# Kernel optimization log

Measured on AMD Instinct MI355X. Metric: run time of the kernel, lower is better.

The kernel has to match this reference:

```python
import jax, jax.numpy as jnp
import numpy as np

B, LQ, LK = 16, 1024, 4096
QD, KD = 512, 512


def setup_inputs() -> dict:
    key = jax.random.key(0)
    ks = jax.random.split(key, 8)
    s = lambda d: 1.0 / np.sqrt(d)
    return {
        "query": jax.random.normal(ks[0], (B, LQ, QD), dtype=jnp.float32),
        "keys": jax.random.normal(ks[1], (B, LK, KD), dtype=jnp.float32),
        "Wq": jax.random.uniform(ks[2], (QD, KD), jnp.float32, -s(QD), s(QD)),
        "bq": jax.random.uniform(ks[3], (KD,), jnp.float32, -s(QD), s(QD)),
        "Wk": jax.random.uniform(ks[4], (KD, KD), jnp.float32, -s(KD), s(KD)),
        "bk": jax.random.uniform(ks[5], (KD,), jnp.float32, -s(KD), s(KD)),
        "Wv": jax.random.uniform(ks[6], (KD, KD), jnp.float32, -s(KD), s(KD)),
        "bv": jax.random.uniform(ks[7], (KD,), jnp.float32, -s(KD), s(KD)),
    }


def reference(query, keys, Wq, bq, Wk, bk, Wv, bv):
    scale = 1.0 / np.sqrt(KD)
    q = query @ Wq + bq                       # [B, LQ, KD]
    k = keys @ Wk + bk                        # [B, LK, KD]
    v = k @ Wv + bv                           # NOTE: value proj applied to projected keys (as in source)
    scores = jnp.einsum('bqd,bkd->bqk', q, k) * scale  # [B, LQ, LK]
    attn = jax.nn.softmax(scores, axis=2)
    context = jnp.einsum('bqk,bkd->bqd', attn, v)      # [B, LQ, KD]
    return context
```

## Files before the change

kernel.cpp:

```cpp
#include <hip/hip_runtime.h>
#include <hip/hip_bf16.h>
#include <stdint.h>


typedef __attribute__((ext_vector_type(8))) short bf16x8;
typedef __attribute__((ext_vector_type(4))) float f32x4;
typedef __attribute__((ext_vector_type(8))) unsigned short ushort8v;
typedef __attribute__((ext_vector_type(4))) unsigned short ushort4v;

__device__ __forceinline__ unsigned short f2bf(float f) {
  union { float f; unsigned int u; } x{f};
  unsigned int r = x.u + 0x7FFFu + ((x.u >> 16) & 1u);
  return (unsigned short)(r >> 16);
}
__device__ __forceinline__ float bf2f(unsigned short h) {
  union { unsigned int u; float f; } x{(unsigned int)h << 16};
  return x.f;
}

#define GLOAD_LDS16(gptr, lptr)                                                  \
  __builtin_amdgcn_global_load_lds((const __attribute__((address_space(1))) void*)(gptr), \
                                   (__attribute__((address_space(3))) void*)(lptr), 16, 0, 0)

__global__ __launch_bounds__(256) void cast_bf16_kernel(const float* __restrict__ in,
                                                        unsigned short* __restrict__ out,
                                                        long n) {
  long i = ((long)blockIdx.x * blockDim.x + threadIdx.x) * 8;
  long stride = (long)gridDim.x * blockDim.x * 8;
  for (; i < n; i += stride) {
    const float4* p = (const float4*)(in + i);
    float4 a = p[0], b = p[1];
    ushort8v o;
    o[0] = f2bf(a.x); o[1] = f2bf(a.y); o[2] = f2bf(a.z); o[3] = f2bf(a.w);
    o[4] = f2bf(b.x); o[5] = f2bf(b.y); o[6] = f2bf(b.z); o[7] = f2bf(b.w);
    *(ushort8v*)(out + i) = o;
  }
}

__global__ __launch_bounds__(256) void transpose_w_kernel(const float* __restrict__ W0,
                                                          const float* __restrict__ W1,
                                                          const float* __restrict__ W2,
                                                          unsigned short* __restrict__ T0,
                                                          unsigned short* __restrict__ T1,
                                                          unsigned short* __restrict__ T2) {
  const float* W = (blockIdx.z == 0) ? W0 : (blockIdx.z == 1) ? W1 : W2;
  unsigned short* T = (blockIdx.z == 0) ? T0 : (blockIdx.z == 1) ? T1 : T2;
  __shared__ float tile[32][33];
  int tx = threadIdx.x & 31, ty = threadIdx.x >> 5;
  int gx = blockIdx.x * 32 + tx;
  int gy0 = blockIdx.y * 32;
#pragma unroll
  for (int i = 0; i < 32; i += 8) tile[ty + i][tx] = W[(size_t)(gy0 + ty + i) * 512 + gx];
  __syncthreads();
  int ox = blockIdx.y * 32 + tx;
  int oy0 = blockIdx.x * 32;
#pragma unroll
  for (int i = 0; i < 32; i += 8)
    T[(size_t)(oy0 + ty + i) * 512 + ox] = f2bf(tile[tx][ty + i]);
}

template <int OUT_MODE>
__global__ __launch_bounds__(256, 2) void gemm_nt(const unsigned short* __restrict__ A,
                                                  const unsigned short* __restrict__ Bt,
                                                  const float* __restrict__ bias,
                                                  void* __restrict__ Cout,
                                                  int M, int N, int K, float scale) {
  __shared__ __align__(16) unsigned short lA[2][128][64];
  __shared__ __align__(16) unsigned short lB[2][128][64];
  const int tid = threadIdx.x;
  const int lane = tid & 63;
  const int wave = tid >> 6;
  const int m0 = blockIdx.y * 128;
  const int n0 = blockIdx.x * 128;

  f32x4 acc[4][4] = {};

  auto stage = [&](int buf, int kt) {
    const int k0 = kt * 64;
#pragma unroll
    for (int p = 0; p < 4; ++p) {
      int c = p * 4 + wave;
      int f = c * 512 + lane * 8;
      int row = f >> 6, col = f & 63;
      const unsigned short* gA = A + (size_t)(m0 + row) * K + (k0 + col);
      const unsigned short* gB = Bt + (size_t)(n0 + row) * K + (k0 + col);
      GLOAD_LDS16(gA, &lA[buf][0][0] + c * 512);
      GLOAD_LDS16(gB, &lB[buf][0][0] + c * 512);
    }
  };

  const int wm = wave >> 1, wn = wave & 1;
  const int lr = lane & 15;
  const int lk = (lane >> 4) << 3;

  const int KT = K >> 6;
  stage(0, 0);
  __syncthreads();
  int cur = 0;
  for (int kt = 0; kt < KT; ++kt) {
    if (kt + 1 < KT) stage(cur ^ 1, kt + 1);
#pragma unroll
    for (int kk = 0; kk < 64; kk += 32) {
      bf16x8 af[4], bfv[4];
#pragma unroll
      for (int i = 0; i < 4; ++i)
        af[i] = *(const bf16x8*)&lA[cur][wm * 64 + i * 16 + lr][kk + lk];
#pragma unroll
      for (int j = 0; j < 4; ++j)
        bfv[j] = *(const bf16x8*)&lB[cur][wn * 64 + j * 16 + lr][kk + lk];
#pragma unroll
      for (int i = 0; i < 4; ++i)
#pragma unroll
        for (int j = 0; j < 4; ++j)
          acc[i][j] = __builtin_amdgcn_mfma_f32_16x16x32_bf16(af[i], bfv[j], acc[i][j], 0, 0, 0);
    }
    __syncthreads();
    cur ^= 1;
  }

  const int ci = lane & 15;
  const int ri = (lane >> 4) * 4;
#pragma unroll
  for (int i = 0; i < 4; ++i) {
#pragma unroll
    for (int j = 0; j < 4; ++j) {
      int gm = m0 + wm * 64 + i * 16 + ri;
      int gn = n0 + wn * 64 + j * 16 + ci;
      float bv_ = bias[gn];
      f32x4 a = acc[i][j];
      if (OUT_MODE == 0) {
        unsigned short* C = (unsigned short*)Cout;
#pragma unroll
        for (int r = 0; r < 4; ++r)
          C[(size_t)(gm + r) * N + gn] = f2bf((a[r] + bv_) * scale);
      } else {
        unsigned short* C = (unsigned short*)Cout;
        int b_ = gm >> 12;
        int ml = gm & 4095;
        ushort4v pk;
#pragma unroll
        for (int r = 0; r < 4; ++r) pk[r] = f2bf((a[r] + bv_) * scale);
        *(ushort4v*)&C[((size_t)b_ * 512 + gn) * 4096 + ml] = pk;
      }
    }
  }
}

__global__ __launch_bounds__(512, 1) void flash_attn(const unsigned short* __restrict__ q,
                                                     const unsigned short* __restrict__ k,
                                                     const unsigned short* __restrict__ vT,
                                                     float* __restrict__ out) {
  __shared__ __align__(16) unsigned short lQ[64 * 512];
  __shared__ __align__(16) unsigned short lP[2][64 * 128];
  __shared__ float redm[64 * 8], reds[64 * 8];
  __shared__ float m_s[64], rs_s[64];

  const int tid = threadIdx.x;
  const int lane = tid & 63;
  const int w = tid >> 6;
  const int g = lane >> 4;
  const int r16 = lane & 15;
  const int bid = blockIdx.x;
  const int b = (bid & 7) * 2 + ((bid >> 3) >> 4);
  const int qt = (bid >> 3) & 15;

  const unsigned short* Qb = q + ((size_t)b * 1024 + qt * 64) * 512;
  const unsigned short* Kb = k + (size_t)b * 4096 * 512;
  const unsigned short* Vb = vT + (size_t)b * 512 * 4096;

#pragma unroll
  for (int i = 0; i < 8; ++i) {
    int byte = (i * 512 + tid) * 16;
    int row = byte >> 10;
    int colB = byte & 1023;
    int srcB = (colB & ~127) | ((colB & 127) ^ ((row & 7) << 4));
    GLOAD_LDS16(Qb + (size_t)row * 512 + (srcB >> 1), (char*)lQ + byte);
  }
  float m_run = -1e30f, l_run = 0.f;
  float rs_reg = 0.f;
  __syncthreads();

  f32x4 acc_o[4][4] = {};
  const int rowK = w * 16 + r16;
  const unsigned short* KrowBase = Kb + (size_t)rowK * 512 + (g << 3);

  for (int t = 0; t < 32; ++t) {
    const int pbuf = t & 1;
    const unsigned short* Krow = KrowBase + (size_t)t * 128 * 512;
    bf16x8 kf[16];
#pragma unroll
    for (int s = 0; s < 16; ++s) kf[s] = *(const bf16x8*)(Krow + s * 32);

    f32x4 accS[4] = {};
#pragma unroll
    for (int s = 0; s < 16; ++s) {
#pragma unroll
      for (int nf = 0; nf < 4; ++nf) {
        int rowQ = nf * 16 + r16;
        int base = s * 64 + (g << 4);
        int colQB = (base & ~127) | ((base & 127) ^ ((rowQ & 7) << 4));
        bf16x8 qf = *(const bf16x8*)((char*)lQ + rowQ * 1024 + colQB);
        accS[nf] = __builtin_amdgcn_mfma_f32_16x16x32_bf16(kf[s], qf, accS[nf], 0, 0, 0);
      }
    }

    bf16x8 vf[4][4];
#pragma unroll
    for (int nf = 0; nf < 4; ++nf) {
      int d = (w << 6) + (nf << 4) + r16;
      const unsigned short* Vrow = Vb + (size_t)d * 4096 + t * 128 + (g << 3);
#pragma unroll
      for (int ks = 0; ks < 4; ++ks) vf[nf][ks] = *(const bf16x8*)(Vrow + (ks << 5));
    }

#pragma unroll
    for (int nf = 0; nf < 4; ++nf) {
      f32x4 s = accS[nf];
      float mx = fmaxf(fmaxf(s[0], s[1]), fmaxf(s[2], s[3]));
      mx = fmaxf(mx, __shfl_xor(mx, 16));
      mx = fmaxf(mx, __shfl_xor(mx, 32));
      if (lane < 16) redm[(nf * 16 + lane) * 8 + w] = mx;
    }
    __syncthreads();
    if (w == 0) {
      f32x4 a = *(const f32x4*)&redm[lane * 8];
      f32x4 a2 = *(const f32x4*)&redm[lane * 8 + 4];
      float tmax = fmaxf(fmaxf(fmaxf(a[0], a[1]), fmaxf(a[2], a[3])),
                         fmaxf(fmaxf(a2[0], a2[1]), fmaxf(a2[2], a2[3])));
      float m_new = fmaxf(m_run, tmax);
      rs_reg = __expf(m_run - m_new);
      m_run = m_new;
      m_s[lane] = m_new;
      rs_s[lane] = rs_reg;
    }
    __syncthreads();
#pragma unroll
    for (int nf = 0; nf < 4; ++nf) {
      int qrow = nf * 16 + r16;
      float mq = m_s[qrow];
      f32x4 s = accS[nf];
      ushort4v pk;
      float sum = 0.f;
#pragma unroll
      for (int rr = 0; rr < 4; ++rr) {
        float p = __expf(s[rr] - mq);
        sum += p;
        pk[rr] = f2bf(p);
      }
      sum += __shfl_xor(sum, 16);
      sum += __shfl_xor(sum, 32);
      if (lane < 16) reds[qrow * 8 + w] = sum;
      int colB = (w * 32 + (g << 3)) ^ ((qrow & 7) << 4);
      *(ushort4v*)((char*)lP[pbuf] + qrow * 256 + colB) = pk;
    }
#pragma unroll
    for (int mf = 0; mf < 4; ++mf) {
      f32x4 rsv = *(const f32x4*)&rs_s[(mf << 4) + (g << 2)];
#pragma unroll
      for (int nf = 0; nf < 4; ++nf)
#pragma unroll
        for (int rr = 0; rr < 4; ++rr) acc_o[mf][nf][rr] *= rsv[rr];
    }
    __syncthreads();
    if (w == 0) {
      f32x4 a = *(const f32x4*)&reds[lane * 8];
      f32x4 a2 = *(const f32x4*)&reds[lane * 8 + 4];
      float tsum = (a[0] + a[1] + a[2] + a[3]) + (a2[0] + a2[1] + a2[2] + a2[3]);
      l_run = l_run * rs_reg + tsum;
    }

#pragma unroll
    for (int ks = 0; ks < 4; ++ks) {
#pragma unroll
      for (int mf = 0; mf < 4; ++mf) {
        int qr = (mf << 4) + r16;
        int colB = ((ks << 6) + (g << 4)) ^ ((qr & 7) << 4);
        bf16x8 ap = *(const bf16x8*)((char*)lP[pbuf] + qr * 256 + colB);
#pragma unroll
        for (int nf = 0; nf < 4; ++nf)
          acc_o[mf][nf] = __builtin_amdgcn_mfma_f32_16x16x32_bf16(ap, vf[nf][ks], acc_o[mf][nf], 0, 0, 0);
      }
    }
  }

  if (w == 0) rs_s[lane] = 1.f / l_run;
  __syncthreads();
#pragma unroll
  for (int mf = 0; mf < 4; ++mf) {
    f32x4 il = *(const f32x4*)&rs_s[(mf << 4) + (g << 2)];
#pragma unroll
    for (int nf = 0; nf < 4; ++nf) {
      int d = (w << 6) + (nf << 4) + r16;
#pragma unroll
      for (int rr = 0; rr < 4; ++rr) {
        int qr = (mf << 4) + (g << 2) + rr;
        out[((size_t)b * 1024 + qt * 64 + qr) * 512 + d] = acc_o[mf][nf][rr] * il[rr];
      }
    }
  }
}

extern "C" void kernel_launch(void* const* d_in, const int* in_sizes, int n_in,
                              void* d_out, int out_size, void* d_ws, size_t ws_size,
                              hipStream_t stream) {
  const float* query = (const float*)d_in[0];
  const float* keys  = (const float*)d_in[1];
  const float* Wq = (const float*)d_in[2];
  const float* bq = (const float*)d_in[3];
  const float* Wk = (const float*)d_in[4];
  const float* bk = (const float*)d_in[5];
  const float* Wv = (const float*)d_in[6];
  const float* bv = (const float*)d_in[7];
  float* out = (float*)d_out;

  char* w = (char*)d_ws;
  unsigned short* query_bf = (unsigned short*)w;
  unsigned short* keys_bf  = (unsigned short*)(w + 16777216);
  unsigned short* q_bf = (unsigned short*)(w + 83886080);
  unsigned short* k_bf = (unsigned short*)(w + 100663296);
  unsigned short* vT   = (unsigned short*)(w + 167772160);
  unsigned short* WqT  = (unsigned short*)(w + 234881024);
  unsigned short* WkT  = WqT + 262144;
  unsigned short* WvT  = WkT + 262144;

  const float scale = 0.04419417382415922f;

  cast_bf16_kernel<<<1024, 256, 0, stream>>>(query, query_bf, 8388608L);
  cast_bf16_kernel<<<2048, 256, 0, stream>>>(keys, keys_bf, 33554432L);
  transpose_w_kernel<<<dim3(16, 16, 3), 256, 0, stream>>>(Wq, Wk, Wv, WqT, WkT, WvT);

  gemm_nt<0><<<dim3(4, 128), 256, 0, stream>>>(query_bf, WqT, bq, q_bf,
                                               16384, 512, 512, scale);
  gemm_nt<0><<<dim3(4, 512), 256, 0, stream>>>(keys_bf, WkT, bk, k_bf,
                                               65536, 512, 512, 1.f);
  gemm_nt<1><<<dim3(4, 512), 256, 0, stream>>>(k_bf, WvT, bv, vT,
                                               65536, 512, 512, 1.f);
  flash_attn<<<256, 512, 0, stream>>>(q_bf, k_bf, vT, out);

  (void)in_sizes; (void)n_in; (void)out_size; (void)ws_size;
}
```

Before: 665.9 us.

## Restructure flash attention around 32x32 MFMA with 32-row query tiles

Reworks the attention kernel to use 32x32x16 bf16 MFMA instead of 16x16x32. Query tiles shrink from 64 to 32 rows and key tiles grow from 128 to 256 rows, which halves the number of outer iterations and doubles the grid to 512 blocks. Launch bounds now request 4 blocks per CU so occupancy can rise. The cost is that each block rereads K and V for only 32 queries, doubling global K/V traffic, in exchange for better CU fill and fewer barrier rounds per key.

```diff
diff --git a/kernel.cpp b/kernel.cpp
--- a/kernel.cpp
+++ b/kernel.cpp
@@ -5,6 +5,7 @@
 
 typedef __attribute__((ext_vector_type(8))) short bf16x8;
 typedef __attribute__((ext_vector_type(4))) float f32x4;
+typedef __attribute__((ext_vector_type(16))) float f32x16;
 typedef __attribute__((ext_vector_type(8))) unsigned short ushort8v;
 typedef __attribute__((ext_vector_type(4))) unsigned short ushort4v;
 
@@ -146,30 +147,31 @@
   }
 }
 
-__global__ __launch_bounds__(512, 1) void flash_attn(const unsigned short* __restrict__ q,
+__global__ __launch_bounds__(512, 4) void flash_attn(const unsigned short* __restrict__ q,
                                                      const unsigned short* __restrict__ k,
                                                      const unsigned short* __restrict__ vT,
                                                      float* __restrict__ out) {
-  __shared__ __align__(16) unsigned short lQ[64 * 512];
-  __shared__ __align__(16) unsigned short lP[2][64 * 128];
-  __shared__ float redm[64 * 8], reds[64 * 8];
-  __shared__ float m_s[64], rs_s[64];
+  __shared__ __align__(16) unsigned short lQ[32 * 512];
+  __shared__ __align__(16) unsigned short lP[2][32 * 256];
+  __shared__ __align__(16) float redm[32 * 8], reds[32 * 8];
+  __shared__ float m_s[32], rs_s[32];
 
   const int tid = threadIdx.x;
   const int lane = tid & 63;
   const int w = tid >> 6;
-  const int g = lane >> 4;
-  const int r16 = lane & 15;
+  const int h = lane >> 5;
+  const int c31 = lane & 31;
   const int bid = blockIdx.x;
-  const int b = (bid & 7) * 2 + ((bid >> 3) >> 4);
-  const int qt = (bid >> 3) & 15;
-
-  const unsigned short* Qb = q + ((size_t)b * 1024 + qt * 64) * 512;
+  const int idx = bid >> 3;
+  const int b = (bid & 7) * 2 + (idx >> 5);
+  const int qt = idx & 31;
+
+  const unsigned short* Qb = q + ((size_t)b * 1024 + qt * 32) * 512;
   const unsigned short* Kb = k + (size_t)b * 4096 * 512;
   const unsigned short* Vb = vT + (size_t)b * 512 * 4096;
 
 #pragma unroll
-  for (int i = 0; i < 8; ++i) {
+  for (int i = 0; i < 4; ++i) {
     int byte = (i * 512 + tid) * 16;
     int row = byte >> 10;
     int colB = byte & 1023;
@@ -180,49 +182,40 @@
   float rs_reg = 0.f;
   __syncthreads();
 
-  f32x4 acc_o[4][4] = {};
-  const int rowK = w * 16 + r16;
-  const unsigned short* KrowBase = Kb + (size_t)rowK * 512 + (g << 3);
-
-  for (int t = 0; t < 32; ++t) {
+  f32x16 acc_o[2] = {};
+  const unsigned short* Krow = Kb + ((size_t)(w * 32 + c31)) * 512 + h * 8;
+  const unsigned short* V0 = Vb + (size_t)((w * 2 + 0) * 32 + c31) * 4096;
+  const unsigned short* V1 = Vb + (size_t)((w * 2 + 1) * 32 + c31) * 4096;
+
+  for (int t = 0; t < 16; ++t) {
     const int pbuf = t & 1;
-    const unsigned short* Krow = KrowBase + (size_t)t * 128 * 512;
-    bf16x8 kf[16];
-#pragma unroll
-    for (int s = 0; s < 16; ++s) kf[s] = *(const bf16x8*)(Krow + s * 32);
-
-    f32x4 accS[4] = {};
-#pragma unroll
-    for (int s = 0; s < 16; ++s) {
-#pragma unroll
-      for (int nf = 0; nf < 4; ++nf) {
-        int rowQ = nf * 16 + r16;
-        int base = s * 64 + (g << 4);
-        int colQB = (base & ~127) | ((base & 127) ^ ((rowQ & 7) << 4));
-        bf16x8 qf = *(const bf16x8*)((char*)lQ + rowQ * 1024 + colQB);
-        accS[nf] = __builtin_amdgcn_mfma_f32_16x16x32_bf16(kf[s], qf, accS[nf], 0, 0, 0);
-      }
-    }
-
-    bf16x8 vf[4][4];
-#pragma unroll
-    for (int nf = 0; nf < 4; ++nf) {
-      int d = (w << 6) + (nf << 4) + r16;
-      const unsigned short* Vrow = Vb + (size_t)d * 4096 + t * 128 + (g << 3);
-#pragma unroll
-      for (int ks = 0; ks < 4; ++ks) vf[nf][ks] = *(const bf16x8*)(Vrow + (ks << 5));
-    }
-
-#pragma unroll
-    for (int nf = 0; nf < 4; ++nf) {
-      f32x4 s = accS[nf];
-      float mx = fmaxf(fmaxf(s[0], s[1]), fmaxf(s[2], s[3]));
-      mx = fmaxf(mx, __shfl_xor(mx, 16));
-      mx = fmaxf(mx, __shfl_xor(mx, 32));
-      if (lane < 16) redm[(nf * 16 + lane) * 8 + w] = mx;
-    }
+    const unsigned short* Kt = Krow + (size_t)t * 256 * 512;
+
+    f32x16 accS = {};
+#pragma unroll
+    for (int sb = 0; sb < 8; ++sb) {
+      bf16x8 kf0 = *(const bf16x8*)(Kt + (sb * 4 + 0) * 16);
+      bf16x8 kf1 = *(const bf16x8*)(Kt + (sb * 4 + 1) * 16);
+      bf16x8 kf2 = *(const bf16x8*)(Kt + (sb * 4 + 2) * 16);
+      bf16x8 kf3 = *(const bf16x8*)(Kt + (sb * 4 + 3) * 16);
+#pragma unroll
+      for (int j = 0; j < 4; ++j) {
+        int s = sb * 4 + j;
+        int base = s * 32 + h * 16;
+        int colQB = (base & ~127) | ((base & 127) ^ ((c31 & 7) << 4));
+        bf16x8 qv = *(const bf16x8*)((char*)lQ + c31 * 1024 + colQB);
+        bf16x8 kf = (j == 0) ? kf0 : (j == 1) ? kf1 : (j == 2) ? kf2 : kf3;
+        accS = __builtin_amdgcn_mfma_f32_32x32x16_bf16(kf, qv, accS, 0, 0, 0);
+      }
+    }
+
+    float mx = accS[0];
+#pragma unroll
+    for (int r = 1; r < 16; ++r) mx = fmaxf(mx, accS[r]);
+    mx = fmaxf(mx, __shfl_xor(mx, 32));
+    if (lane < 32) redm[lane * 8 + w] = mx;
     __syncthreads();
-    if (w == 0) {
+    if (w == 0 && lane < 32) {
       f32x4 a = *(const f32x4*)&redm[lane * 8];
       f32x4 a2 = *(const f32x4*)&redm[lane * 8 + 4];
       float tmax = fmaxf(fmaxf(fmaxf(a[0], a[1]), fmaxf(a[2], a[3])),
@@ -234,67 +227,71 @@
       rs_s[lane] = rs_reg;
     }
     __syncthreads();
-#pragma unroll
-    for (int nf = 0; nf < 4; ++nf) {
-      int qrow = nf * 16 + r16;
-      float mq = m_s[qrow];
-      f32x4 s = accS[nf];
-      ushort4v pk;
+    {
+      float mq = m_s[c31];
       float sum = 0.f;
 #pragma unroll
-      for (int rr = 0; rr < 4; ++rr) {
-        float p = __expf(s[rr] - mq);
-        sum += p;
-        pk[rr] = f2bf(p);
-      }
-      sum += __shfl_xor(sum, 16);
+      for (int j = 0; j < 4; ++j) {
+        ushort4v pk;
+#pragma unroll
+        for (int i = 0; i < 4; ++i) {
+          float p = __expf(accS[j * 4 + i] - mq);
+          sum += p;
+          pk[i] = f2bf(p);
+        }
+        int colB = (w * 64 + j * 16 + h * 8) ^ ((c31 & 7) << 4);
+        *(ushort4v*)((char*)lP[pbuf] + c31 * 512 + colB) = pk;
+      }
       sum += __shfl_xor(sum, 32);
-      if (lane < 16) reds[qrow * 8 + w] = sum;
-      int colB = (w * 32 + (g << 3)) ^ ((qrow & 7) << 4);
-      *(ushort4v*)((char*)lP[pbuf] + qrow * 256 + colB) = pk;
-    }
-#pragma unroll
-    for (int mf = 0; mf < 4; ++mf) {
-      f32x4 rsv = *(const f32x4*)&rs_s[(mf << 4) + (g << 2)];
-#pragma unroll
-      for (int nf = 0; nf < 4; ++nf)
-#pragma unroll
-        for (int rr = 0; rr < 4; ++rr) acc_o[mf][nf][rr] *= rsv[rr];
+      if (lane < 32) reds[lane * 8 + w] = sum;
+    }
+#pragma unroll
+    for (int j = 0; j < 4; ++j) {
+      f32x4 rv = *(const f32x4*)&rs_s[8 * j + 4 * h];
+#pragma unroll
+      for (int i = 0; i < 4; ++i) {
+        acc_o[0][j * 4 + i] *= rv[i];
+        acc_o[1][j * 4 + i] *= rv[i];
+      }
     }
     __syncthreads();
-    if (w == 0) {
+    if (w == 0 && lane < 32) {
       f32x4 a = *(const f32x4*)&reds[lane * 8];
       f32x4 a2 = *(const f32x4*)&reds[lane * 8 + 4];
       float tsum = (a[0] + a[1] + a[2] + a[3]) + (a2[0] + a2[1] + a2[2] + a2[3]);
       l_run = l_run * rs_reg + tsum;
     }
 
-#pragma unroll
-    for (int ks = 0; ks < 4; ++ks) {
-#pragma unroll
-      for (int mf = 0; mf < 4; ++mf) {
-        int qr = (mf << 4) + r16;
-        int colB = ((ks << 6) + (g << 4)) ^ ((qr & 7) << 4);
-        bf16x8 ap = *(const bf16x8*)((char*)lP[pbuf] + qr * 256 + colB);
-#pragma unroll
-        for (int nf = 0; nf < 4; ++nf)
-          acc_o[mf][nf] = __builtin_amdgcn_mfma_f32_16x16x32_bf16(ap, vf[nf][ks], acc_o[mf][nf], 0, 0, 0);
-      }
-    }
-  }
-
-  if (w == 0) rs_s[lane] = 1.f / l_run;
+    const unsigned short* Vt0 = V0 + t * 256 + h * 8;
+    const unsigned short* Vt1 = V1 + t * 256 + h * 8;
+#pragma unroll
+    for (int kb = 0; kb < 8; ++kb) {
+#pragma unroll
+      for (int u = 0; u < 2; ++u) {
+        int ks = kb * 2 + u;
+        bf16x8 vf0 = *(const bf16x8*)(Vt0 + ks * 16);
+        bf16x8 vf1 = *(const bf16x8*)(Vt1 + ks * 16);
+        int colB = (ks * 32 + h * 16) ^ ((c31 & 7) << 4);
+        bf16x8 pa = *(const bf16x8*)((char*)lP[pbuf] + c31 * 512 + colB);
+        acc_o[0] = __builtin_amdgcn_mfma_f32_32x32x16_bf16(pa, vf0, acc_o[0], 0, 0, 0);
+        acc_o[1] = __builtin_amdgcn_mfma_f32_32x32x16_bf16(pa, vf1, acc_o[1], 0, 0, 0);
+      }
+    }
+  }
+
+  if (w == 0 && lane < 32) rs_s[lane] = 1.f / l_run;
   __syncthreads();
-#pragma unroll
-  for (int mf = 0; mf < 4; ++mf) {
-    f32x4 il = *(const f32x4*)&rs_s[(mf << 4) + (g << 2)];
-#pragma unroll
-    for (int nf = 0; nf < 4; ++nf) {
-      int d = (w << 6) + (nf << 4) + r16;
-#pragma unroll
-      for (int rr = 0; rr < 4; ++rr) {
-        int qr = (mf << 4) + (g << 2) + rr;
-        out[((size_t)b * 1024 + qt * 64 + qr) * 512 + d] = acc_o[mf][nf][rr] * il[rr];
+  {
+    const int q0 = qt * 32;
+#pragma unroll
+    for (int j = 0; j < 4; ++j) {
+      f32x4 il = *(const f32x4*)&rs_s[8 * j + 4 * h];
+#pragma unroll
+      for (int i = 0; i < 4; ++i) {
+        int qr = 8 * j + 4 * h + i;
+        float* orow = out + ((size_t)b * 1024 + q0 + qr) * 512;
+        orow[(w * 2 + 0) * 32 + c31] = acc_o[0][j * 4 + i] * il[i];
+        orow[(w * 2 + 1) * 32 + c31] = acc_o[1][j * 4 + i] * il[i];
       }
     }
   }
@@ -335,7 +332,7 @@
                                                65536, 512, 512, 1.f);
   gemm_nt<1><<<dim3(4, 512), 256, 0, stream>>>(k_bf, WvT, bv, vT,
                                                65536, 512, 512, 1.f);
-  flash_attn<<<256, 512, 0, stream>>>(q_bf, k_bf, vT, out);
+  flash_attn<<<512, 512, 0, stream>>>(q_bf, k_bf, vT, out);
 
   (void)in_sizes; (void)n_in; (void)out_size; (void)ws_size;
 }
```

Result: slower. 866.4 us (+30.1%).

## Apply value projection after attention and fuse projected-key transpose into key GEMM

Applied to the files above, without the earlier changes.

Because softmax rows sum to one, attn @ (k Wv + bv) equals (attn @ k) Wv + bv. The value projection therefore moves after attention: flash attention runs on the projected keys (transposed copy written by the key GEMM), emits a bf16 context, and a small 16384-row GEMM applies Wv and bv. This replaces the 65536-row value GEMM with a quarter-size one and adds a dual-write epilogue to the key GEMM, plus s_setprio hints around the MFMA loops. The extra bf16 rounding of the context before the final projection adds some precision risk.

```diff
diff --git a/kernel.cpp b/kernel.cpp
--- a/kernel.cpp
+++ b/kernel.cpp
@@ -64,6 +64,7 @@
                                                   const unsigned short* __restrict__ Bt,
                                                   const float* __restrict__ bias,
                                                   void* __restrict__ Cout,
+                                                  void* __restrict__ Cout2,
                                                   int M, int N, int K, float scale) {
   __shared__ __align__(16) unsigned short lA[2][128][64];
   __shared__ __align__(16) unsigned short lB[2][128][64];
@@ -133,14 +134,24 @@
 #pragma unroll
         for (int r = 0; r < 4; ++r)
           C[(size_t)(gm + r) * N + gn] = f2bf((a[r] + bv_) * scale);
+      } else if (OUT_MODE == 2) {
+        float* C = (float*)Cout;
+#pragma unroll
+        for (int r = 0; r < 4; ++r)
+          C[(size_t)(gm + r) * N + gn] = (a[r] + bv_) * scale;
       } else {
         unsigned short* C = (unsigned short*)Cout;
+        unsigned short* C2 = (unsigned short*)Cout2;
+        ushort4v pk;
+#pragma unroll
+        for (int r = 0; r < 4; ++r) {
+          unsigned short hv = f2bf((a[r] + bv_) * scale);
+          C[(size_t)(gm + r) * N + gn] = hv;
+          pk[r] = hv;
+        }
         int b_ = gm >> 12;
         int ml = gm & 4095;
-        ushort4v pk;
-#pragma unroll
-        for (int r = 0; r < 4; ++r) pk[r] = f2bf((a[r] + bv_) * scale);
-        *(ushort4v*)&C[((size_t)b_ * 512 + gn) * 4096 + ml] = pk;
+        *(ushort4v*)&C2[((size_t)b_ * 512 + gn) * 4096 + ml] = pk;
       }
     }
   }
@@ -148,8 +159,8 @@
 
 __global__ __launch_bounds__(512, 1) void flash_attn(const unsigned short* __restrict__ q,
                                                      const unsigned short* __restrict__ k,
-                                                     const unsigned short* __restrict__ vT,
-                                                     float* __restrict__ out) {
+                                                     const unsigned short* __restrict__ kT,
+                                                     unsigned short* __restrict__ ctx0) {
   __shared__ __align__(16) unsigned short lQ[64 * 512];
   __shared__ __align__(16) unsigned short lP[2][64 * 128];
   __shared__ float redm[64 * 8], reds[64 * 8];
@@ -166,7 +177,7 @@
 
   const unsigned short* Qb = q + ((size_t)b * 1024 + qt * 64) * 512;
   const unsigned short* Kb = k + (size_t)b * 4096 * 512;
-  const unsigned short* Vb = vT + (size_t)b * 512 * 4096;
+  const unsigned short* Vb = kT + (size_t)b * 512 * 4096;
 
 #pragma unroll
   for (int i = 0; i < 8; ++i) {
@@ -192,6 +203,7 @@
     for (int s = 0; s < 16; ++s) kf[s] = *(const bf16x8*)(Krow + s * 32);
 
     f32x4 accS[4] = {};
+    __builtin_amdgcn_s_setprio(1);
 #pragma unroll
     for (int s = 0; s < 16; ++s) {
 #pragma unroll
@@ -203,6 +215,7 @@
         accS[nf] = __builtin_amdgcn_mfma_f32_16x16x32_bf16(kf[s], qf, accS[nf], 0, 0, 0);
       }
     }
+    __builtin_amdgcn_s_setprio(0);
 
     bf16x8 vf[4][4];
 #pragma unroll
@@ -269,6 +282,7 @@
       l_run = l_run * rs_reg + tsum;
     }
 
+    __builtin_amdgcn_s_setprio(1);
 #pragma unroll
     for (int ks = 0; ks < 4; ++ks) {
 #pragma unroll
@@ -281,6 +295,7 @@
           acc_o[mf][nf] = __builtin_amdgcn_mfma_f32_16x16x32_bf16(ap, vf[nf][ks], acc_o[mf][nf], 0, 0, 0);
       }
     }
+    __builtin_amdgcn_s_setprio(0);
   }
 
   if (w == 0) rs_s[lane] = 1.f / l_run;
@@ -294,7 +309,7 @@
 #pragma unroll
       for (int rr = 0; rr < 4; ++rr) {
         int qr = (mf << 4) + (g << 2) + rr;
-        out[((size_t)b * 1024 + qt * 64 + qr) * 512 + d] = acc_o[mf][nf][rr] * il[rr];
+        ctx0[((size_t)b * 1024 + qt * 64 + qr) * 512 + d] = f2bf(acc_o[mf][nf][rr] * il[rr]);
       }
     }
   }
@@ -316,9 +331,10 @@
   char* w = (char*)d_ws;
   unsigned short* query_bf = (unsigned short*)w;
   unsigned short* keys_bf  = (unsigned short*)(w + 16777216);
+  unsigned short* ctx0     = (unsigned short*)w;
   unsigned short* q_bf = (unsigned short*)(w + 83886080);
   unsigned short* k_bf = (unsigned short*)(w + 100663296);
-  unsigned short* vT   = (unsigned short*)(w + 167772160);
+  unsigned short* kT   = (unsigned short*)(w + 167772160);
   unsigned short* WqT  = (unsigned short*)(w + 234881024);
   unsigned short* WkT  = WqT + 262144;
   unsigned short* WvT  = WkT + 262144;
@@ -329,13 +345,13 @@
   cast_bf16_kernel<<<2048, 256, 0, stream>>>(keys, keys_bf, 33554432L);
   transpose_w_kernel<<<dim3(16, 16, 3), 256, 0, stream>>>(Wq, Wk, Wv, WqT, WkT, WvT);
 
-  gemm_nt<0><<<dim3(4, 128), 256, 0, stream>>>(query_bf, WqT, bq, q_bf,
+  gemm_nt<0><<<dim3(4, 128), 256, 0, stream>>>(query_bf, WqT, bq, q_bf, nullptr,
                                                16384, 512, 512, scale);
-  gemm_nt<0><<<dim3(4, 512), 256, 0, stream>>>(keys_bf, WkT, bk, k_bf,
+  gemm_nt<3><<<dim3(4, 512), 256, 0, stream>>>(keys_bf, WkT, bk, k_bf, kT,
                                                65536, 512, 512, 1.f);
-  gemm_nt<1><<<dim3(4, 512), 256, 0, stream>>>(k_bf, WvT, bv, vT,
-                                               65536, 512, 512, 1.f);
-  flash_attn<<<256, 512, 0, stream>>>(q_bf, k_bf, vT, out);
+  flash_attn<<<256, 512, 0, stream>>>(q_bf, k_bf, kT, ctx0);
+  gemm_nt<2><<<dim3(4, 128), 256, 0, stream>>>(ctx0, WvT, bv, out, nullptr,
+                                               16384, 512, 512, 1.f);
 
   (void)in_sizes; (void)n_in; (void)out_size; (void)ws_size;
 }
```

New measurement: 629.1 us. -5.5%, faster.
